# Performance work log

Hardware: AMD Instinct MI355X
Metric: run time of the kernel (lower is better)

Reference implementation:

```python
import jax, jax.numpy as jnp
import numpy as np

BN_EPS = 1e-5


def setup_inputs() -> dict:
    key = jax.random.key(0)
    ks = jax.random.split(key, 8)
    N, Cin, Cout, D, H, W = 4, 512, 256, 256, 128, 128
    feat_ffm = jax.random.normal(ks[0], (N, Cin, H, W), dtype=jnp.float32)
    coarse_x = jax.random.normal(ks[1], (N, D, H, W), dtype=jnp.float32)
    # conv1: 1x1, no bias; BN (eval mode: running stats); conv2: 1x1 with bias
    w1 = jax.random.normal(ks[2], (Cout, Cin), dtype=jnp.float32) * (1.0 / np.sqrt(Cin))
    bn_gamma = jnp.ones((Cout,), dtype=jnp.float32)
    bn_beta = jnp.zeros((Cout,), dtype=jnp.float32)
    bn_mean = jax.random.normal(ks[3], (Cout,), dtype=jnp.float32) * 0.1
    bn_var = jax.random.uniform(ks[4], (Cout,), dtype=jnp.float32, minval=0.5, maxval=1.5)
    w2 = jax.random.normal(ks[5], (Cout, Cout), dtype=jnp.float32) * (1.0 / np.sqrt(Cout))
    b2 = jnp.zeros((Cout,), dtype=jnp.float32)
    return {"feat_ffm": feat_ffm, "coarse_x": coarse_x, "w1": w1,
            "bn_gamma": bn_gamma, "bn_beta": bn_beta, "bn_mean": bn_mean,
            "bn_var": bn_var, "w2": w2, "b2": b2}


def reference(feat_ffm, coarse_x, w1, bn_gamma, bn_beta, bn_mean, bn_var, w2, b2):
    N, D, H, W = coarse_x.shape
    # conv1 (1x1) + BN(eval) + ReLU; Dropout2d is identity in eval mode
    x = jnp.einsum('nihw,oi->nohw', feat_ffm, w1)
    scale = bn_gamma * jax.lax.rsqrt(bn_var + BN_EPS)
    x = x * scale[None, :, None, None] + (bn_beta - bn_mean * scale)[None, :, None, None]
    x = jax.nn.relu(x)  # [N, C, H, W]
    C = x.shape[1]
    q = coarse_x.reshape(N, D, H * W)          # proj_query / proj_value
    k = x.reshape(N, C, H * W)                 # proj_key (pre-permute)
    energy = jnp.einsum('nds,ncs->ndc', q, k)  # [N, D, C]
    energy_new = jnp.max(energy, axis=-1, keepdims=True) - energy
    attention = jax.nn.softmax(energy_new, axis=-1)        # [N, D, C]
    out = jnp.einsum('ndc,nds->ncs', attention, q)         # attention^T @ value
    out = out.reshape(N, C, H, W)
    out = jnp.einsum('nchw,oc->nohw', out, w2) + b2[None, :, None, None]
    return out
```

## Files before the change

### kernel.cpp

```cpp
#include <hip/hip_runtime.h>


#define S_DIM 16384
#define C_DIM 256
#define CIN 512

typedef unsigned short u16;
typedef __attribute__((ext_vector_type(8))) short bf16x8;
typedef __attribute__((ext_vector_type(4))) float f32x4;

__device__ __forceinline__ u16 f2bf(float x) {
    unsigned u = __float_as_uint(x);
    u += 0x7fff + ((u >> 16) & 1);
    return (u16)(u >> 16);
}
__device__ __forceinline__ float bf2f(u16 h) {
    return __uint_as_float(((unsigned)h) << 16);
}
__device__ __forceinline__ void gld16(const u16* g, u16* l) {
    __builtin_amdgcn_global_load_lds((const __attribute__((address_space(1))) void*)g,
                                     (__attribute__((address_space(3))) void*)l, 16, 0, 0);
}

__global__ __launch_bounds__(128) void fold_split_w1(
    const float* __restrict__ w1, const float* __restrict__ gamma,
    const float* __restrict__ beta, const float* __restrict__ mean,
    const float* __restrict__ var, u16* __restrict__ whi, u16* __restrict__ wlo,
    float* __restrict__ b1) {
    int o = blockIdx.x;
    float sc = gamma[o] * rsqrtf(var[o] + 1e-5f);
    for (int i = threadIdx.x; i < CIN; i += 128) {
        float v = w1[o * CIN + i] * sc;
        u16 h = f2bf(v);
        whi[o * CIN + i] = h;
        wlo[o * CIN + i] = f2bf(v - bf2f(h));
    }
    if (threadIdx.x == 0) b1[o] = beta[o] - mean[o] * sc;
}

__global__ __launch_bounds__(256) void zero_kernel(float* __restrict__ p, int n) {
    int i = blockIdx.x * 256 + threadIdx.x;
    if (i < n) p[i] = 0.0f;
}

__global__ __launch_bounds__(256) void split_q(const float* __restrict__ src,
                                               u16* __restrict__ qhi, u16* __restrict__ qlo) {
    size_t i = (size_t)blockIdx.x * 256 + threadIdx.x;
    for (size_t c = i; c < 4194304u; c += 1048576u) {
        float4 v = ((const float4*)src)[c];
        float vv[4] = {v.x, v.y, v.z, v.w};
        u16 h[4], l[4];
#pragma unroll
        for (int j = 0; j < 4; ++j) {
            h[j] = f2bf(vv[j]);
            l[j] = f2bf(vv[j] - bf2f(h[j]));
        }
        *(uint2*)&qhi[c * 4] = *(uint2*)h;
        *(uint2*)&qlo[c * 4] = *(uint2*)l;
    }
}

__global__ __launch_bounds__(256) void transpose_feat(const float* __restrict__ src,
                                                      u16* __restrict__ dhi,
                                                      u16* __restrict__ dlo) {
    int s0 = blockIdx.x * 64;
    int i0 = blockIdx.y * 64;
    size_t sb = (size_t)blockIdx.z * 8388608;
    __shared__ u16 Th[64][65], Tl[64][65];
    int t = threadIdx.x;
#pragma unroll
    for (int p = 0; p < 4; ++p) {
        int idx = t + p * 256;
        int row = idx >> 4, c4 = (idx & 15) * 4;
        float4 v = *(const float4*)&src[sb + (size_t)(i0 + row) * S_DIM + s0 + c4];
        float vv[4] = {v.x, v.y, v.z, v.w};
#pragma unroll
        for (int j = 0; j < 4; ++j) {
            u16 h = f2bf(vv[j]);
            Th[c4 + j][row] = h;
            Tl[c4 + j][row] = f2bf(vv[j] - bf2f(h));
        }
    }
    __syncthreads();
#pragma unroll
    for (int p = 0; p < 2; ++p) {
        int idx = t + p * 256;
        int row = idx >> 3, c8 = (idx & 7) * 8;
        u16 hh[8], ll[8];
#pragma unroll
        for (int j = 0; j < 8; ++j) { hh[j] = Th[row][c8 + j]; ll[j] = Tl[row][c8 + j]; }
        *(uint4*)&dhi[sb + (size_t)(s0 + row) * CIN + i0 + c8] = *(uint4*)hh;
        *(uint4*)&dlo[sb + (size_t)(s0 + row) * CIN + i0 + c8] = *(uint4*)ll;
    }
}

__global__ __launch_bounds__(256) void transpose_q(const u16* __restrict__ src,
                                                   u16* __restrict__ dst) {
    int s0 = blockIdx.x * 64;
    int d0 = blockIdx.y * 64;
    size_t sb = (size_t)blockIdx.z * 4194304;
    __shared__ u16 T[64][65];
    int t = threadIdx.x;
#pragma unroll
    for (int p = 0; p < 2; ++p) {
        int idx = t + p * 256;
        int row = idx >> 3, c8 = (idx & 7) * 8;
        u16 v[8];
        *(uint4*)v = *(const uint4*)&src[sb + (size_t)(d0 + row) * S_DIM + s0 + c8];
#pragma unroll
        for (int j = 0; j < 8; ++j) T[c8 + j][row] = v[j];
    }
    __syncthreads();
#pragma unroll
    for (int p = 0; p < 2; ++p) {
        int idx = t + p * 256;
        int row = idx >> 3, c8 = (idx & 7) * 8;
        u16 v[8];
#pragma unroll
        for (int j = 0; j < 8; ++j) v[j] = T[row][c8 + j];
        *(uint4*)&dst[sb + (size_t)(s0 + row) * C_DIM + d0 + c8] = *(uint4*)v;
    }
}

template <int SPLIT, int EPI>
__global__ __launch_bounds__(256) void gemm_nt(
    const u16* __restrict__ Ah, const u16* __restrict__ Al, long aStride,
    const u16* __restrict__ Bh, const u16* __restrict__ Bl, long bStride,
    int K, int kLen,
    const float* __restrict__ bias,
    float* __restrict__ outF, long oStrideF,
    u16* __restrict__ oHi, u16* __restrict__ oLo, long oStrideH,
    int ldOut) {
    __shared__ u16 AhS[4096];
    __shared__ u16 BhS[4096];
    __shared__ u16 AlS[SPLIT == 3 ? 4096 : 8];
    __shared__ u16 BlS[SPLIT == 3 ? 4096 : 8];

    int m0, n0, kBeg;
    if (EPI == 0) {
        kBeg = blockIdx.x * kLen;
        m0 = (blockIdx.y >> 1) * 128;
        n0 = (blockIdx.y & 1) * 128;
    } else {
        kBeg = 0;
        n0 = blockIdx.x * 128;
        m0 = blockIdx.y * 128;
    }
    int bz = blockIdx.z;
    int tid = threadIdx.x;
    int wave = tid >> 6, lane = tid & 63;

    int c0 = wave * 128 + lane;
    int c1 = c0 + 64;
    int r0 = c0 >> 2, k0 = (c0 & 3) * 8;
    int r1 = c1 >> 2, k1 = (c1 & 3) * 8;
    const u16* gAh0 = Ah + (size_t)bz * aStride + (size_t)(m0 + r0) * K + kBeg + k0;
    const u16* gAh1 = Ah + (size_t)bz * aStride + (size_t)(m0 + r1) * K + kBeg + k1;
    const u16* gBh0 = Bh + (size_t)bz * bStride + (size_t)(n0 + r0) * K + kBeg + k0;
    const u16* gBh1 = Bh + (size_t)bz * bStride + (size_t)(n0 + r1) * K + kBeg + k1;
    const u16 *gAl0 = nullptr, *gAl1 = nullptr, *gBl0 = nullptr, *gBl1 = nullptr;
    if (SPLIT == 3) {
        gAl0 = Al + (size_t)bz * aStride + (size_t)(m0 + r0) * K + kBeg + k0;
        gAl1 = Al + (size_t)bz * aStride + (size_t)(m0 + r1) * K + kBeg + k1;
        gBl0 = Bl + (size_t)bz * bStride + (size_t)(n0 + r0) * K + kBeg + k0;
        gBl1 = Bl + (size_t)bz * bStride + (size_t)(n0 + r1) * K + kBeg + k1;
    }

    int quad = lane >> 4, l15 = lane & 15;
    int wm = wave >> 1, wn = wave & 1;
    int aBase = (wm * 64 + l15) * 32 + quad * 8;
    int bBase = (wn * 64 + l15) * 32 + quad * 8;

    f32x4 zero = {0.f, 0.f, 0.f, 0.f};
    f32x4 acc[4][4];
#pragma unroll
    for (int i = 0; i < 4; ++i)
#pragma unroll
        for (int j = 0; j < 4; ++j) acc[i][j] = zero;

    for (int kb = 0; kb < kLen; kb += 32) {
        __syncthreads();
        gld16(gAh0, AhS + c0 * 8);
        gld16(gAh1, AhS + c1 * 8);
        gld16(gBh0, BhS + c0 * 8);
        gld16(gBh1, BhS + c1 * 8);
        gAh0 += 32; gAh1 += 32; gBh0 += 32; gBh1 += 32;
        if (SPLIT == 3) {
            gld16(gAl0, AlS + c0 * 8);
            gld16(gAl1, AlS + c1 * 8);
            gld16(gBl0, BlS + c0 * 8);
            gld16(gBl1, BlS + c1 * 8);
            gAl0 += 32; gAl1 += 32; gBl0 += 32; gBl1 += 32;
        }
        __syncthreads();

        bf16x8 a_h[4], b_h[4], a_l[4], b_l[4];
#pragma unroll
        for (int t = 0; t < 4; ++t) {
            a_h[t] = *(const bf16x8*)&AhS[aBase + t * 512];
            b_h[t] = *(const bf16x8*)&BhS[bBase + t * 512];
            if (SPLIT == 3) {
                a_l[t] = *(const bf16x8*)&AlS[aBase + t * 512];
                b_l[t] = *(const bf16x8*)&BlS[bBase + t * 512];
            }
        }
#pragma unroll
        for (int mt = 0; mt < 4; ++mt)
#pragma unroll
            for (int nt = 0; nt < 4; ++nt) {
                acc[mt][nt] = __builtin_amdgcn_mfma_f32_16x16x32_bf16(a_h[mt], b_h[nt], acc[mt][nt], 0, 0, 0);
                if (SPLIT == 3) {
                    acc[mt][nt] = __builtin_amdgcn_mfma_f32_16x16x32_bf16(a_h[mt], b_l[nt], acc[mt][nt], 0, 0, 0);
                    acc[mt][nt] = __builtin_amdgcn_mfma_f32_16x16x32_bf16(a_l[mt], b_h[nt], acc[mt][nt], 0, 0, 0);
                }
            }
    }

#pragma unroll
    for (int mt = 0; mt < 4; ++mt) {
#pragma unroll
        for (int r = 0; r < 4; ++r) {
            int row = m0 + wm * 64 + mt * 16 + quad * 4 + r;
            float bi = (EPI != 0) ? bias[row] : 0.f;
#pragma unroll
            for (int nt = 0; nt < 4; ++nt) {
                int cc = n0 + wn * 64 + nt * 16 + l15;
                float v = acc[mt][nt][r];
                if (EPI == 0) {
                    atomicAdd(&outF[(size_t)bz * oStrideF + (size_t)row * ldOut + cc], v);
                } else if (EPI == 1) {
                    v = fmaxf(v + bi, 0.f);
                    u16 h = f2bf(v);
                    size_t o = (size_t)bz * oStrideH + (size_t)row * ldOut + cc;
                    oHi[o] = h;
                    oLo[o] = f2bf(v - bf2f(h));
                } else {
                    outF[(size_t)bz * oStrideF + (size_t)row * ldOut + cc] = v + bi;
                }
            }
        }
    }
}

__global__ __launch_bounds__(256) void softmax_kernel(const float* __restrict__ E,
                                                      float* __restrict__ att) {
    int row = blockIdx.x;
    int c = threadIdx.x;
    float v = E[(size_t)row * C_DIM + c];
    float m = v;
#pragma unroll
    for (int o = 32; o > 0; o >>= 1) m = fminf(m, __shfl_xor(m, o, 64));
    __shared__ float red[4];
    __shared__ float red2[4];
    int lane = c & 63, wid = c >> 6;
    if (lane == 0) red[wid] = m;
    __syncthreads();
    m = fminf(fminf(red[0], red[1]), fminf(red[2], red[3]));
    float e = expf(m - v);
    float s = e;
#pragma unroll
    for (int o = 32; o > 0; o >>= 1) s += __shfl_xor(s, o, 64);
    if (lane == 0) red2[wid] = s;
    __syncthreads();
    s = red2[0] + red2[1] + red2[2] + red2[3];
    att[(size_t)row * C_DIM + c] = e / s;
}

__global__ __launch_bounds__(256) void m2h_kernel(const float* __restrict__ w2,
                                                  const float* __restrict__ att,
                                                  u16* __restrict__ M2h) {
    int t = blockIdx.x * 256 + threadIdx.x;
    int d = t & 255, o = (t >> 8) & 255, n = t >> 16;
    const float4* wr = (const float4*)(w2 + (size_t)o * C_DIM);
    const float4* ar = (const float4*)(att + ((size_t)n * C_DIM + d) * C_DIM);
    float s = 0.0f;
#pragma unroll 4
    for (int c4 = 0; c4 < 64; ++c4) {
        float4 w = wr[c4];
        float4 a = ar[c4];
        s += w.x * a.x + w.y * a.y + w.z * a.z + w.w * a.w;
    }
    M2h[((size_t)n * C_DIM + o) * C_DIM + d] = f2bf(s);
}

extern "C" void kernel_launch(void* const* d_in, const int* in_sizes, int n_in,
                              void* d_out, int out_size, void* d_ws, size_t ws_size,
                              hipStream_t stream) {
    const float* feat   = (const float*)d_in[0];
    const float* coarse = (const float*)d_in[1];
    const float* w1     = (const float*)d_in[2];
    const float* gamma  = (const float*)d_in[3];
    const float* beta   = (const float*)d_in[4];
    const float* mean   = (const float*)d_in[5];
    const float* var    = (const float*)d_in[6];
    const float* w2     = (const float*)d_in[7];
    const float* b2     = (const float*)d_in[8];
    float* out = (float*)d_out;

    char* base = (char*)d_ws;
    u16* qhi  = (u16*)(base);
    u16* qlo  = (u16*)(base + 33554432);
    u16* khi  = (u16*)(base + 67108864);
    u16* klo  = (u16*)(base + 100663296);
    u16* fThi = (u16*)(base + 134217728);
    u16* fTlo = (u16*)(base + 167772160);
    u16* qThi = (u16*)(base + 134217728);
    float* E   = (float*)(base + 201326592);
    float* att = (float*)(base + 202375168);
    u16* M2h   = (u16*)(base + 203423744);
    u16* w1hi  = (u16*)(base + 203948032);
    u16* w1lo  = (u16*)(base + 204210176);
    float* b1  = (float*)(base + 204472320);

    fold_split_w1<<<256, 128, 0, stream>>>(w1, gamma, beta, mean, var, w1hi, w1lo, b1);
    split_q<<<4096, 256, 0, stream>>>(coarse, qhi, qlo);
    zero_kernel<<<1024, 256, 0, stream>>>(E, 262144);

    for (int pair = 0; pair < 2; ++pair) {
        transpose_feat<<<dim3(256, 8, 2), 256, 0, stream>>>(feat + (size_t)pair * 16777216,
                                                            fThi, fTlo);
        gemm_nt<3, 1><<<dim3(128, 2, 2), 256, 0, stream>>>(
            w1hi, w1lo, 0, fThi, fTlo, 8388608, CIN, CIN, b1,
            nullptr, 0, khi + (size_t)pair * 8388608, klo + (size_t)pair * 8388608,
            4194304, S_DIM);
    }

    gemm_nt<3, 0><<<dim3(32, 4, 4), 256, 0, stream>>>(
        qhi, qlo, 4194304, khi, klo, 4194304, S_DIM, 512, nullptr,
        E, 65536, nullptr, nullptr, 0, C_DIM);

    softmax_kernel<<<1024, 256, 0, stream>>>(E, att);
    m2h_kernel<<<1024, 256, 0, stream>>>(w2, att, M2h);
    transpose_q<<<dim3(256, 4, 4), 256, 0, stream>>>(qhi, qThi);

    gemm_nt<1, 2><<<dim3(128, 2, 4), 256, 0, stream>>>(
        M2h, nullptr, 65536, qThi, nullptr, 4194304, C_DIM, C_DIM, b2,
        out, 4194304, nullptr, nullptr, 0, S_DIM);
}
```

Baseline: 496.8 us.

## Merge prep kernels, replace split-K atomics with partial buffers, fuse reduce+softmax+transpose

Folds the weight fold, q split and feature transpose into one prep kernel over a larger workspace, so the conv1 GEMM runs as a single launch over all four batches instead of two pairs. The split-K energy GEMM now writes per-split partial tiles instead of float atomics, which also removes the zero-fill kernel. A post kernel sums the 32 partials before the softmax, and the same launch also transposes q. This cuts launch count and atomic traffic, at the cost of more workspace memory and an extra 32-way reduction read.

Measured after the change: 496.2 us. Within noise of the previous version (-0.1%).

```diff
diff --git a/kernel.cpp b/kernel.cpp
--- a/kernel.cpp
+++ b/kernel.cpp
@@ -22,103 +22,70 @@
                                      (__attribute__((address_space(3))) void*)l, 16, 0, 0);
 }
 
-__global__ __launch_bounds__(128) void fold_split_w1(
+__global__ __launch_bounds__(256) void prep_kernel(
+    const float* __restrict__ feat, const float* __restrict__ coarse,
     const float* __restrict__ w1, const float* __restrict__ gamma,
     const float* __restrict__ beta, const float* __restrict__ mean,
-    const float* __restrict__ var, u16* __restrict__ whi, u16* __restrict__ wlo,
-    float* __restrict__ b1) {
-    int o = blockIdx.x;
-    float sc = gamma[o] * rsqrtf(var[o] + 1e-5f);
-    for (int i = threadIdx.x; i < CIN; i += 128) {
-        float v = w1[o * CIN + i] * sc;
-        u16 h = f2bf(v);
-        whi[o * CIN + i] = h;
-        wlo[o * CIN + i] = f2bf(v - bf2f(h));
-    }
-    if (threadIdx.x == 0) b1[o] = beta[o] - mean[o] * sc;
-}
-
-__global__ __launch_bounds__(256) void zero_kernel(float* __restrict__ p, int n) {
-    int i = blockIdx.x * 256 + threadIdx.x;
-    if (i < n) p[i] = 0.0f;
-}
-
-__global__ __launch_bounds__(256) void split_q(const float* __restrict__ src,
-                                               u16* __restrict__ qhi, u16* __restrict__ qlo) {
-    size_t i = (size_t)blockIdx.x * 256 + threadIdx.x;
-    for (size_t c = i; c < 4194304u; c += 1048576u) {
-        float4 v = ((const float4*)src)[c];
-        float vv[4] = {v.x, v.y, v.z, v.w};
-        u16 h[4], l[4];
-#pragma unroll
-        for (int j = 0; j < 4; ++j) {
-            h[j] = f2bf(vv[j]);
-            l[j] = f2bf(vv[j] - bf2f(h[j]));
-        }
-        *(uint2*)&qhi[c * 4] = *(uint2*)h;
-        *(uint2*)&qlo[c * 4] = *(uint2*)l;
-    }
-}
-
-__global__ __launch_bounds__(256) void transpose_feat(const float* __restrict__ src,
-                                                      u16* __restrict__ dhi,
-                                                      u16* __restrict__ dlo) {
-    int s0 = blockIdx.x * 64;
-    int i0 = blockIdx.y * 64;
-    size_t sb = (size_t)blockIdx.z * 8388608;
+    const float* __restrict__ var,
+    u16* __restrict__ fThi, u16* __restrict__ fTlo,
+    u16* __restrict__ qhi, u16* __restrict__ qlo,
+    u16* __restrict__ w1hi, u16* __restrict__ w1lo, float* __restrict__ b1) {
     __shared__ u16 Th[64][65], Tl[64][65];
+    int b = blockIdx.x;
     int t = threadIdx.x;
-#pragma unroll
-    for (int p = 0; p < 4; ++p) {
-        int idx = t + p * 256;
-        int row = idx >> 4, c4 = (idx & 15) * 4;
-        float4 v = *(const float4*)&src[sb + (size_t)(i0 + row) * S_DIM + s0 + c4];
-        float vv[4] = {v.x, v.y, v.z, v.w};
-#pragma unroll
-        for (int j = 0; j < 4; ++j) {
-            u16 h = f2bf(vv[j]);
-            Th[c4 + j][row] = h;
-            Tl[c4 + j][row] = f2bf(vv[j] - bf2f(h));
-        }
-    }
-    __syncthreads();
-#pragma unroll
-    for (int p = 0; p < 2; ++p) {
-        int idx = t + p * 256;
-        int row = idx >> 3, c8 = (idx & 7) * 8;
-        u16 hh[8], ll[8];
-#pragma unroll
-        for (int j = 0; j < 8; ++j) { hh[j] = Th[row][c8 + j]; ll[j] = Tl[row][c8 + j]; }
-        *(uint4*)&dhi[sb + (size_t)(s0 + row) * CIN + i0 + c8] = *(uint4*)hh;
-        *(uint4*)&dlo[sb + (size_t)(s0 + row) * CIN + i0 + c8] = *(uint4*)ll;
-    }
-}
-
-__global__ __launch_bounds__(256) void transpose_q(const u16* __restrict__ src,
-                                                   u16* __restrict__ dst) {
-    int s0 = blockIdx.x * 64;
-    int d0 = blockIdx.y * 64;
-    size_t sb = (size_t)blockIdx.z * 4194304;
-    __shared__ u16 T[64][65];
-    int t = threadIdx.x;
-#pragma unroll
-    for (int p = 0; p < 2; ++p) {
-        int idx = t + p * 256;
-        int row = idx >> 3, c8 = (idx & 7) * 8;
-        u16 v[8];
-        *(uint4*)v = *(const uint4*)&src[sb + (size_t)(d0 + row) * S_DIM + s0 + c8];
-#pragma unroll
-        for (int j = 0; j < 8; ++j) T[c8 + j][row] = v[j];
-    }
-    __syncthreads();
-#pragma unroll
-    for (int p = 0; p < 2; ++p) {
-        int idx = t + p * 256;
-        int row = idx >> 3, c8 = (idx & 7) * 8;
-        u16 v[8];
-#pragma unroll
-        for (int j = 0; j < 8; ++j) v[j] = T[row][c8 + j];
-        *(uint4*)&dst[sb + (size_t)(s0 + row) * C_DIM + d0 + c8] = *(uint4*)v;
+    if (b < 8192) {
+        int s0 = (b & 255) * 64;
+        int i0 = ((b >> 8) & 7) * 64;
+        size_t sb = (size_t)(b >> 11) * 8388608;
+#pragma unroll
+        for (int p = 0; p < 4; ++p) {
+            int idx = t + p * 256;
+            int row = idx >> 4, c4 = (idx & 15) * 4;
+            float4 v = *(const float4*)&feat[sb + (size_t)(i0 + row) * S_DIM + s0 + c4];
+            float vv[4] = {v.x, v.y, v.z, v.w};
+#pragma unroll
+            for (int j = 0; j < 4; ++j) {
+                u16 h = f2bf(vv[j]);
+                Th[c4 + j][row] = h;
+                Tl[c4 + j][row] = f2bf(vv[j] - bf2f(h));
+            }
+        }
+        __syncthreads();
+#pragma unroll
+        for (int p = 0; p < 2; ++p) {
+            int idx = t + p * 256;
+            int row = idx >> 3, c8 = (idx & 7) * 8;
+            u16 hh[8], ll[8];
+#pragma unroll
+            for (int j = 0; j < 8; ++j) { hh[j] = Th[row][c8 + j]; ll[j] = Tl[row][c8 + j]; }
+            *(uint4*)&fThi[sb + (size_t)(s0 + row) * CIN + i0 + c8] = *(uint4*)hh;
+            *(uint4*)&fTlo[sb + (size_t)(s0 + row) * CIN + i0 + c8] = *(uint4*)ll;
+        }
+    } else if (b < 12288) {
+        size_t i = (size_t)(b - 8192) * 256 + t;
+        for (size_t c = i; c < 4194304u; c += 1048576u) {
+            float4 v = ((const float4*)coarse)[c];
+            float vv[4] = {v.x, v.y, v.z, v.w};
+            u16 h[4], l[4];
+#pragma unroll
+            for (int j = 0; j < 4; ++j) {
+                h[j] = f2bf(vv[j]);
+                l[j] = f2bf(vv[j] - bf2f(h[j]));
+            }
+            *(uint2*)&qhi[c * 4] = *(uint2*)h;
+            *(uint2*)&qlo[c * 4] = *(uint2*)l;
+        }
+    } else {
+        int o = (b - 12288) * 16 + (t >> 4);
+        int lane16 = t & 15;
+        float sc = gamma[o] * rsqrtf(var[o] + 1e-5f);
+        for (int i = lane16; i < CIN; i += 16) {
+            float v = w1[o * CIN + i] * sc;
+            u16 h = f2bf(v);
+            w1hi[o * CIN + i] = h;
+            w1lo[o * CIN + i] = f2bf(v - bf2f(h));
+        }
+        if (lane16 == 0) b1[o] = beta[o] - mean[o] * sc;
     }
 }
 
@@ -216,6 +183,8 @@
             }
     }
 
+    float* Ce = nullptr;
+    if (EPI == 0) Ce = outF + ((size_t)(blockIdx.x * gridDim.z + bz)) * 65536;
 #pragma unroll
     for (int mt = 0; mt < 4; ++mt) {
 #pragma unroll
@@ -227,7 +196,7 @@
                 int cc = n0 + wn * 64 + nt * 16 + l15;
                 float v = acc[mt][nt][r];
                 if (EPI == 0) {
-                    atomicAdd(&outF[(size_t)bz * oStrideF + (size_t)row * ldOut + cc], v);
+                    Ce[(size_t)row * ldOut + cc] = v;
                 } else if (EPI == 1) {
                     v = fmaxf(v + bi, 0.f);
                     u16 h = f2bf(v);
@@ -242,28 +211,60 @@
     }
 }
 
-__global__ __launch_bounds__(256) void softmax_kernel(const float* __restrict__ E,
-                                                      float* __restrict__ att) {
-    int row = blockIdx.x;
-    int c = threadIdx.x;
-    float v = E[(size_t)row * C_DIM + c];
-    float m = v;
-#pragma unroll
-    for (int o = 32; o > 0; o >>= 1) m = fminf(m, __shfl_xor(m, o, 64));
-    __shared__ float red[4];
-    __shared__ float red2[4];
-    int lane = c & 63, wid = c >> 6;
-    if (lane == 0) red[wid] = m;
-    __syncthreads();
-    m = fminf(fminf(red[0], red[1]), fminf(red[2], red[3]));
-    float e = expf(m - v);
-    float s = e;
-#pragma unroll
-    for (int o = 32; o > 0; o >>= 1) s += __shfl_xor(s, o, 64);
-    if (lane == 0) red2[wid] = s;
-    __syncthreads();
-    s = red2[0] + red2[1] + red2[2] + red2[3];
-    att[(size_t)row * C_DIM + c] = e / s;
+__global__ __launch_bounds__(256) void post_kernel(const float* __restrict__ Ep,
+                                                   float* __restrict__ att,
+                                                   const u16* __restrict__ qhi,
+                                                   u16* __restrict__ qT) {
+    __shared__ u16 T[64][65];
+    __shared__ float red[4], red2[4];
+    int b = blockIdx.x;
+    int t = threadIdx.x;
+    if (b < 1024) {
+        int n = b >> 8, d = b & 255;
+        const float* p = Ep + ((size_t)n * 256 + d) * 256 + t;
+        float v = 0.f;
+#pragma unroll 8
+        for (int s = 0; s < 32; ++s) v += p[(size_t)s * 262144];
+        float m = v;
+#pragma unroll
+        for (int o = 32; o > 0; o >>= 1) m = fminf(m, __shfl_xor(m, o, 64));
+        int lane = t & 63, wid = t >> 6;
+        if (lane == 0) red[wid] = m;
+        __syncthreads();
+        m = fminf(fminf(red[0], red[1]), fminf(red[2], red[3]));
+        float e = expf(m - v);
+        float s = e;
+#pragma unroll
+        for (int o = 32; o > 0; o >>= 1) s += __shfl_xor(s, o, 64);
+        if (lane == 0) red2[wid] = s;
+        __syncthreads();
+        s = red2[0] + red2[1] + red2[2] + red2[3];
+        att[(size_t)b * 256 + t] = e / s;
+    } else {
+        int i = b - 1024;
+        int s0 = (i & 255) * 64;
+        int d0 = ((i >> 8) & 3) * 64;
+        size_t sb = (size_t)(i >> 10) * 4194304;
+#pragma unroll
+        for (int p = 0; p < 2; ++p) {
+            int idx = t + p * 256;
+            int row = idx >> 3, c8 = (idx & 7) * 8;
+            u16 v[8];
+            *(uint4*)v = *(const uint4*)&qhi[sb + (size_t)(d0 + row) * S_DIM + s0 + c8];
+#pragma unroll
+            for (int j = 0; j < 8; ++j) T[c8 + j][row] = v[j];
+        }
+        __syncthreads();
+#pragma unroll
+        for (int p = 0; p < 2; ++p) {
+            int idx = t + p * 256;
+            int row = idx >> 3, c8 = (idx & 7) * 8;
+            u16 v[8];
+#pragma unroll
+            for (int j = 0; j < 8; ++j) v[j] = T[row][c8 + j];
+            *(uint4*)&qT[sb + (size_t)(s0 + row) * C_DIM + d0 + c8] = *(uint4*)v;
+        }
+    }
 }
 
 __global__ __launch_bounds__(256) void m2h_kernel(const float* __restrict__ w2,
@@ -298,42 +299,36 @@
     float* out = (float*)d_out;
 
     char* base = (char*)d_ws;
-    u16* qhi  = (u16*)(base);
-    u16* qlo  = (u16*)(base + 33554432);
-    u16* khi  = (u16*)(base + 67108864);
-    u16* klo  = (u16*)(base + 100663296);
-    u16* fThi = (u16*)(base + 134217728);
-    u16* fTlo = (u16*)(base + 167772160);
-    u16* qThi = (u16*)(base + 134217728);
-    float* E   = (float*)(base + 201326592);
-    float* att = (float*)(base + 202375168);
-    u16* M2h   = (u16*)(base + 203423744);
-    u16* w1hi  = (u16*)(base + 203948032);
-    u16* w1lo  = (u16*)(base + 204210176);
-    float* b1  = (float*)(base + 204472320);
-
-    fold_split_w1<<<256, 128, 0, stream>>>(w1, gamma, beta, mean, var, w1hi, w1lo, b1);
-    split_q<<<4096, 256, 0, stream>>>(coarse, qhi, qlo);
-    zero_kernel<<<1024, 256, 0, stream>>>(E, 262144);
-
-    for (int pair = 0; pair < 2; ++pair) {
-        transpose_feat<<<dim3(256, 8, 2), 256, 0, stream>>>(feat + (size_t)pair * 16777216,
-                                                            fThi, fTlo);
-        gemm_nt<3, 1><<<dim3(128, 2, 2), 256, 0, stream>>>(
-            w1hi, w1lo, 0, fThi, fTlo, 8388608, CIN, CIN, b1,
-            nullptr, 0, khi + (size_t)pair * 8388608, klo + (size_t)pair * 8388608,
-            4194304, S_DIM);
-    }
+    u16* qhi   = (u16*)(base);
+    u16* qlo   = (u16*)(base + 33554432);
+    u16* khi   = (u16*)(base + 67108864);
+    u16* klo   = (u16*)(base + 100663296);
+    u16* fThi  = (u16*)(base + 134217728);
+    u16* fTlo  = (u16*)(base + 201326592);
+    u16* qT    = (u16*)(base + 268435456);
+    float* Ep  = (float*)(base + 301989888);
+    float* att = (float*)(base + 335544320);
+    u16* M2h   = (u16*)(base + 336592896);
+    u16* w1hi  = (u16*)(base + 337117184);
+    u16* w1lo  = (u16*)(base + 337379328);
+    float* b1  = (float*)(base + 337641472);
+
+    prep_kernel<<<12304, 256, 0, stream>>>(feat, coarse, w1, gamma, beta, mean, var,
+                                           fThi, fTlo, qhi, qlo, w1hi, w1lo, b1);
+
+    gemm_nt<3, 1><<<dim3(128, 2, 4), 256, 0, stream>>>(
+        w1hi, w1lo, 0, fThi, fTlo, 8388608, CIN, CIN, b1,
+        nullptr, 0, khi, klo, 4194304, S_DIM);
 
     gemm_nt<3, 0><<<dim3(32, 4, 4), 256, 0, stream>>>(
         qhi, qlo, 4194304, khi, klo, 4194304, S_DIM, 512, nullptr,
-        E, 65536, nullptr, nullptr, 0, C_DIM);
-
-    softmax_kernel<<<1024, 256, 0, stream>>>(E, att);
+        Ep, 65536, nullptr, nullptr, 0, C_DIM);
+
+    post_kernel<<<5120, 256, 0, stream>>>(Ep, att, qhi, qT);
+
     m2h_kernel<<<1024, 256, 0, stream>>>(w2, att, M2h);
-    transpose_q<<<dim3(256, 4, 4), 256, 0, stream>>>(qhi, qThi);
 
     gemm_nt<1, 2><<<dim3(128, 2, 4), 256, 0, stream>>>(
-        M2h, nullptr, 65536, qThi, nullptr, 4194304, C_DIM, C_DIM, b2,
+        M2h, nullptr, 65536, qT, nullptr, 4194304, C_DIM, C_DIM, b2,
         out, 4194304, nullptr, nullptr, 0, S_DIM);
 }
```
